# Kernel tuning notes

Hardware: AMD Instinct MI355X
Metric: run time of the kernel (lower is better)

The kernel has to match this reference:

```python
import jax, jax.numpy as jnp
import numpy as np

B, T, D = 2, 2048, 2048
N_HEAD, N_KV_HEAD = 16, 4
HEAD_DIM = D // N_HEAD  # 128
N_REP = N_HEAD // N_KV_HEAD  # 4
ROPE_THETA = 10000.0
EPS = float(jnp.finfo(jnp.float32).eps)  # torch.nn.RMSNorm default eps


def setup_inputs() -> dict:
    key = jax.random.key(0)
    ks = jax.random.split(key, 6)
    s = 0.02
    return {
        "x": jax.random.normal(ks[0], (B, T, D), jnp.float32),
        "wq": jax.random.normal(ks[1], (N_HEAD * HEAD_DIM, D), jnp.float32) * s,
        "wk": jax.random.normal(ks[2], (N_KV_HEAD * HEAD_DIM, D), jnp.float32) * s,
        "wv": jax.random.normal(ks[3], (N_KV_HEAD * HEAD_DIM, D), jnp.float32) * s,
        "wo": jax.random.normal(ks[4], (D, D), jnp.float32) * s,
        "q_norm_w": jnp.ones((HEAD_DIM,), jnp.float32),
        "k_norm_w": jnp.ones((HEAD_DIM,), jnp.float32),
    }


def _rope(x):
    # x: (B, T, H, hd). Llama/Qwen complex-pair RoPE on consecutive pairs.
    t = x.shape[1]
    hd = x.shape[-1]
    inv_freq = 1.0 / (ROPE_THETA ** (jnp.arange(0, hd, 2, dtype=jnp.float32) / hd))
    ang = jnp.arange(t, dtype=jnp.float32)[:, None] * inv_freq[None, :]  # (T, hd/2)
    cos = jnp.cos(ang)[None, :, None, :]
    sin = jnp.sin(ang)[None, :, None, :]
    xr = x[..., 0::2]
    xi = x[..., 1::2]
    or_ = xr * cos - xi * sin
    oi_ = xr * sin + xi * cos
    return jnp.stack([or_, oi_], axis=-1).reshape(x.shape)


def _rmsnorm(x, w):
    var = jnp.mean(jnp.square(x), axis=-1, keepdims=True)
    return x * jax.lax.rsqrt(var + EPS) * w


def reference(x, wq, wk, wv, wo, q_norm_w, k_norm_w):
    b, t, d = x.shape
    xq = (x @ wq.T).reshape(b, t, N_HEAD, HEAD_DIM)
    xk = (x @ wk.T).reshape(b, t, N_KV_HEAD, HEAD_DIM)
    xv = (x @ wv.T).reshape(b, t, N_KV_HEAD, HEAD_DIM)
    xq = _rope(xq)
    xk = _rope(xk)
    # repeat_kv: (B,T,KV,hd) -> (B,T,KV*n_rep,hd)
    xk = jnp.repeat(xk, N_REP, axis=2)
    xv = jnp.repeat(xv, N_REP, axis=2)
    # (B, H, T, hd)
    xq = xq.transpose(0, 2, 1, 3)
    xk = xk.transpose(0, 2, 1, 3)
    xv = xv.transpose(0, 2, 1, 3)
    xq = _rmsnorm(xq, q_norm_w)
    xk = _rmsnorm(xk, k_norm_w)
    scale = 1.0 / np.sqrt(HEAD_DIM)
    scores = jnp.einsum("bhqd,bhkd->bhqk", xq, xk) * scale
    causal = jnp.tril(jnp.ones((t, t), bool))
    scores = jnp.where(causal[None, None], scores, -jnp.inf)
    attn = jax.nn.softmax(scores, axis=-1)
    y = jnp.einsum("bhqk,bhkd->bhqd", attn, xv)
    y = y.transpose(0, 2, 1, 3).reshape(b, t, d)
    return y @ wo.T
```

## Files before the change

kernel.cpp:

```cpp
#include <hip/hip_runtime.h>
#include <hip/hip_bf16.h>
#include <math.h>

typedef __attribute__((ext_vector_type(8))) short bf16x8;
typedef __attribute__((ext_vector_type(4))) float f32x4;
typedef __attribute__((ext_vector_type(4))) unsigned int u32x4;

#define DEV static __device__ __forceinline__

constexpr int TT   = 2048;
constexpr int DDIM = 2048;
constexpr int QKVN = 3072;
constexpr int MROWS = 4096;
constexpr float RSCALE = 0.08838834764831845f;
constexpr float LOG2E  = 1.4426950408889634f;
constexpr float SC2    = RSCALE * LOG2E;
constexpr float REPS   = 1.1920928955078125e-07f;

DEV unsigned short f2b(float f) {
  union { float f; unsigned int u; } v; v.f = f;
  unsigned int u = v.u;
  return (unsigned short)((u + 0x7fffu + ((u >> 16) & 1u)) >> 16);
}
DEV float b2f(unsigned short h) {
  union { unsigned int u; float f; } v; v.u = ((unsigned int)h) << 16;
  return v.f;
}
DEV f32x4 mfma16(bf16x8 a, bf16x8 b, f32x4 c) {
  return __builtin_amdgcn_mfma_f32_16x16x32_bf16(a, b, c, 0, 0, 0);
}
DEV void gload_lds16(const void* g, void* l) {
  __builtin_amdgcn_global_load_lds(
      (const __attribute__((address_space(1))) unsigned int*)g,
      (__attribute__((address_space(3))) unsigned int*)l, 16, 0, 0);
}

__global__ __launch_bounds__(256) void cvt_kernel(const float* __restrict__ in,
                                                  unsigned short* __restrict__ out,
                                                  int n4) {
  int i = blockIdx.x * 256 + threadIdx.x;
  if (i < n4) {
    float4 v = ((const float4*)in)[i];
    ushort4 o;
    o.x = f2b(v.x); o.y = f2b(v.y); o.z = f2b(v.z); o.w = f2b(v.w);
    ((ushort4*)out)[i] = o;
  }
}

template <typename CT>
__global__ __launch_bounds__(256) void gemm_bt(const unsigned short* __restrict__ A,
                                               const unsigned short* __restrict__ B,
                                               CT* __restrict__ C,
                                               int M, int N, int K) {
  __shared__ unsigned short As[128 * 32];
  __shared__ unsigned short Bs[128 * 32];
  const int tid = threadIdx.x;
  const int l = tid & 63, w = tid >> 6;
  const int wr = w >> 1, wc = w & 1;
  const long bm = (long)blockIdx.y * 128, bn = (long)blockIdx.x * 128;

  const int r0 = tid >> 2;
  const int c0 = (tid & 3) * 8;
  const unsigned short* Ag0 = A + (bm + r0) * (long)K + c0;
  const unsigned short* Ag1 = A + (bm + r0 + 64) * (long)K + c0;
  const unsigned short* Bg0 = B + (bn + r0) * (long)K + c0;
  const unsigned short* Bg1 = B + (bn + r0 + 64) * (long)K + c0;
  char* lA = (char*)As + w * 1024;
  char* lB = (char*)Bs + w * 1024;

  f32x4 acc[4][4];
#pragma unroll
  for (int m = 0; m < 4; ++m)
#pragma unroll
    for (int n = 0; n < 4; ++n) acc[m][n] = f32x4{0.f, 0.f, 0.f, 0.f};

  const int lr = l & 15;
  const int lk = (l >> 4) * 8;

  for (int k0 = 0; k0 < K; k0 += 32) {
    gload_lds16(Ag0 + k0, lA);
    gload_lds16(Ag1 + k0, lA + 4096);
    gload_lds16(Bg0 + k0, lB);
    gload_lds16(Bg1 + k0, lB + 4096);
    __syncthreads();
    bf16x8 af[4], bfr[4];
#pragma unroll
    for (int m = 0; m < 4; ++m)
      af[m] = *(const bf16x8*)(As + (wr * 64 + m * 16 + lr) * 32 + lk);
#pragma unroll
    for (int n = 0; n < 4; ++n)
      bfr[n] = *(const bf16x8*)(Bs + (wc * 64 + n * 16 + lr) * 32 + lk);
#pragma unroll
    for (int m = 0; m < 4; ++m)
#pragma unroll
      for (int n = 0; n < 4; ++n)
        acc[m][n] = mfma16(af[m], bfr[n], acc[m][n]);
    __syncthreads();
  }

#pragma unroll
  for (int m = 0; m < 4; ++m)
#pragma unroll
    for (int n = 0; n < 4; ++n)
#pragma unroll
      for (int r = 0; r < 4; ++r) {
        long row = bm + wr * 64 + m * 16 + (l >> 4) * 4 + r;
        long col = bn + wc * 64 + n * 16 + (l & 15);
        float val = acc[m][n][r];
        if constexpr (sizeof(CT) == 2)
          ((unsigned short*)C)[row * N + col] = f2b(val);
        else
          ((float*)C)[row * N + col] = val;
      }
}

__global__ __launch_bounds__(256) void rope_norm_kernel(unsigned short* __restrict__ qkv,
                                                        const float* __restrict__ qw,
                                                        const float* __restrict__ kw) {
  const int slot = blockIdx.x * 4 + (threadIdx.x >> 6);
  const int l = threadIdx.x & 63;
  const int bt = slot / 20;
  const int hs = slot - bt * 20;
  const int t = bt & (TT - 1);
  const bool isq = hs < 16;
  const int col0 = isq ? hs * 128 : 2048 + (hs - 16) * 128;
  const float* w = isq ? qw : kw;
  unsigned short* p = qkv + (long)bt * QKVN + col0;

  unsigned int pr = *(const unsigned int*)(p + 2 * l);
  float xr = b2f((unsigned short)(pr & 0xffffu));
  float xi = b2f((unsigned short)(pr >> 16));

  float ang = (float)t * exp2f(-0.207620509f * (float)l);
  float s = sinf(ang), c = cosf(ang);
  float orr = xr * c - xi * s;
  float oii = xr * s + xi * c;

  float ss = orr * orr + oii * oii;
#pragma unroll
  for (int d = 1; d < 64; d <<= 1) ss += __shfl_xor(ss, d);
  float sc = rsqrtf(ss * (1.f / 128.f) + REPS);

  unsigned int outw = ((unsigned int)f2b(oii * sc * w[2 * l + 1]) << 16) |
                      (unsigned int)f2b(orr * sc * w[2 * l]);
  *(unsigned int*)(p + 2 * l) = outw;
}

__global__ __launch_bounds__(256) void fattn_kernel(const unsigned short* __restrict__ qkv,
                                                    unsigned short* __restrict__ y) {
  const int qb = (int)gridDim.x - 1 - (int)blockIdx.x;
  const int bh = blockIdx.y;
  const int b = bh >> 4, h = bh & 15;
  const unsigned short* base = qkv + (long)b * TT * QKVN;
  const unsigned short* Qp = base + h * 128;
  const unsigned short* Kp = base + 2048 + (h >> 2) * 128;
  const unsigned short* Vp = base + 2560 + (h >> 2) * 128;
  const int tid = threadIdx.x;
  const int l = tid & 63, w = tid >> 6;
  const int lr = l & 15, lg = l >> 4;
  const int qrow = qb * 64 + w * 16;

  __shared__ char KsB[2][16384];
  __shared__ char VtB[2][16384];
  __shared__ unsigned short Ps[4][16][72];

  bf16x8 qf[4];
  {
    const unsigned short* qp = Qp + (long)(qrow + lr) * QKVN + lg * 8;
#pragma unroll
    for (int c = 0; c < 4; ++c) qf[c] = *(const bf16x8*)(qp + c * 32);
  }

  const int krow0 = tid >> 4;
  const int kcolb = ((tid & 15) * 16) ^ ((krow0 & 7) << 4);
  const unsigned short* Kg = Kp + (long)krow0 * QKVN + (kcolb >> 1);
  const int vm = tid & 15;
  const unsigned short* Vg = Vp + (long)(tid >> 4) * QKVN + vm * 8;
  int vwoff[8];
#pragma unroll
  for (int j = 0; j < 8; ++j) {
    int d = vm * 8 + j;
    vwoff[j] = d * 128 + (((((d >> 1) ^ (d >> 3)) & 7) << 4));
  }
  const int lgk = ((lr & 7) << 4);

  f32x4 o[8];
#pragma unroll
  for (int n = 0; n < 8; ++n) o[n] = f32x4{0.f, 0.f, 0.f, 0.f};
  float mrow[4], lsum[4];
#pragma unroll
  for (int r = 0; r < 4; ++r) { mrow[r] = -__builtin_inff(); lsum[r] = 0.f; }

  const int ntiles = qb + 1;
  u32x4 vr[4];

  {
    char* kdst = KsB[0] + (w * 64) * 16;
#pragma unroll
    for (int i = 0; i < 4; ++i)
      gload_lds16(Kg + (long)16 * i * QKVN, kdst + i * 4096);
#pragma unroll
    for (int i = 0; i < 4; ++i)
      vr[i] = *(const u32x4*)(Vg + (long)16 * i * QKVN);
    asm volatile("s_waitcnt vmcnt(0)" ::: "memory");
    char* vt = VtB[0];
#pragma unroll
    for (int i = 0; i < 4; ++i) {
      int kv2 = 2 * ((tid >> 4) + 16 * i);
      const unsigned short* tv = (const unsigned short*)&vr[i];
#pragma unroll
      for (int j = 0; j < 8; ++j) {
        int base128 = (vm * 8 + j) * 128;
        int swz = vwoff[j] - base128;
        *(unsigned short*)(vt + base128 + (kv2 ^ swz)) = tv[j];
      }
    }
    asm volatile("s_waitcnt lgkmcnt(0)" ::: "memory");
    __builtin_amdgcn_s_barrier();
  }

  int cur = 0;
  for (int it = 0; it < ntiles; ++it) {
    const int kv0 = it * 64;
    const int nxt = cur ^ 1;
    const bool pfn = (it + 1 < ntiles);

    if (pfn) {
      const long adv = (long)(it + 1) * 64 * QKVN;
      char* kdst = KsB[nxt] + (w * 64) * 16;
#pragma unroll
      for (int i = 0; i < 4; ++i)
        gload_lds16(Kg + adv + (long)16 * i * QKVN, kdst + i * 4096);
#pragma unroll
      for (int i = 0; i < 4; ++i)
        vr[i] = *(const u32x4*)(Vg + adv + (long)16 * i * QKVN);
    }

    const char* KsC = KsB[cur];
    const char* VtC = VtB[cur];
    f32x4 sb[4];
#pragma unroll
    for (int kb = 0; kb < 4; ++kb) {
      if (kv0 + kb * 16 <= qrow + 15) {
        f32x4 s = f32x4{0.f, 0.f, 0.f, 0.f};
#pragma unroll
        for (int c = 0; c < 4; ++c) {
          bf16x8 kf = *(const bf16x8*)(KsC + (kb * 16 + lr) * 256 +
                                       ((16 * lg + 64 * c) ^ lgk));
          s = mfma16(qf[c], kf, s);
        }
        sb[kb] = s;
      } else {
        sb[kb] = f32x4{-__builtin_inff(), -__builtin_inff(),
                       -__builtin_inff(), -__builtin_inff()};
      }
    }

    float rmax[4];
#pragma unroll
    for (int r = 0; r < 4; ++r) rmax[r] = -__builtin_inff();
#pragma unroll
    for (int kb = 0; kb < 4; ++kb) {
      int kcol = kv0 + kb * 16 + lr;
#pragma unroll
      for (int r = 0; r < 4; ++r) {
        int qr = qrow + lg * 4 + r;
        if (kcol > qr) sb[kb][r] = -__builtin_inff();
        rmax[r] = fmaxf(rmax[r], sb[kb][r]);
      }
    }
#pragma unroll
    for (int r = 0; r < 4; ++r)
#pragma unroll
      for (int d = 1; d < 16; d <<= 1)
        rmax[r] = fmaxf(rmax[r], __shfl_xor(rmax[r], d));

    float alpha[4];
#pragma unroll
    for (int r = 0; r < 4; ++r) {
      float mn = fmaxf(mrow[r], rmax[r] * SC2);
      alpha[r] = exp2f(mrow[r] - mn);
      mrow[r] = mn;
    }
    float rsum[4] = {0.f, 0.f, 0.f, 0.f};
#pragma unroll
    for (int kb = 0; kb < 4; ++kb)
#pragma unroll
      for (int r = 0; r < 4; ++r) {
        float pv = exp2f(sb[kb][r] * SC2 - mrow[r]);
        rsum[r] += pv;
        Ps[w][lg * 4 + r][kb * 16 + lr] = f2b(pv);
      }
#pragma unroll
    for (int r = 0; r < 4; ++r) {
#pragma unroll
      for (int d = 1; d < 16; d <<= 1) rsum[r] += __shfl_xor(rsum[r], d);
      lsum[r] = lsum[r] * alpha[r] + rsum[r];
    }
#pragma unroll
    for (int n = 0; n < 8; ++n)
#pragma unroll
      for (int r = 0; r < 4; ++r) o[n][r] *= alpha[r];

    asm volatile("s_waitcnt lgkmcnt(0)" ::: "memory");
    __builtin_amdgcn_sched_barrier(0);

#pragma unroll
    for (int kc = 0; kc < 2; ++kc) {
      if (kv0 + kc * 32 <= qrow + 15) {
        bf16x8 pf = *(const bf16x8*)(&Ps[w][lr][kc * 32 + lg * 8]);
#pragma unroll
        for (int n = 0; n < 8; ++n) {
          int d = n * 16 + lr;
          int swz = (((d >> 1) ^ (d >> 3)) & 7) << 4;
          bf16x8 vf = *(const bf16x8*)(VtC + d * 128 +
                                       ((kc * 64 + 16 * lg) ^ swz));
          o[n] = mfma16(pf, vf, o[n]);
        }
      }
    }

    if (pfn) {
      asm volatile("s_waitcnt vmcnt(0)" ::: "memory");
      char* vt = VtB[nxt];
#pragma unroll
      for (int i = 0; i < 4; ++i) {
        int kv2 = 2 * ((tid >> 4) + 16 * i);
        const unsigned short* tv = (const unsigned short*)&vr[i];
#pragma unroll
        for (int j = 0; j < 8; ++j) {
          int base128 = (vm * 8 + j) * 128;
          int swz = vwoff[j] - base128;
          *(unsigned short*)(vt + base128 + (kv2 ^ swz)) = tv[j];
        }
      }
      asm volatile("s_waitcnt lgkmcnt(0)" ::: "memory");
      __builtin_amdgcn_s_barrier();
    }
    cur = nxt;
  }

  float inv[4];
#pragma unroll
  for (int r = 0; r < 4; ++r) inv[r] = 1.f / lsum[r];
  unsigned short* yp = y + (long)(b * TT + qrow) * DDIM + h * 128;
#pragma unroll
  for (int n = 0; n < 8; ++n)
#pragma unroll
    for (int r = 0; r < 4; ++r)
      yp[(long)(lg * 4 + r) * DDIM + n * 16 + lr] = f2b(o[n][r] * inv[r]);
}

extern "C" void kernel_launch(void* const* d_in, const int* in_sizes, int n_in,
                              void* d_out, int out_size, void* d_ws, size_t ws_size,
                              hipStream_t stream) {
  const float* x  = (const float*)d_in[0];
  const float* wq = (const float*)d_in[1];
  const float* wk = (const float*)d_in[2];
  const float* wv = (const float*)d_in[3];
  const float* wo = (const float*)d_in[4];
  const float* qw = (const float*)d_in[5];
  const float* kw = (const float*)d_in[6];
  float* out = (float*)d_out;

  unsigned short* xb   = (unsigned short*)d_ws;
  unsigned short* wcat = xb + (size_t)MROWS * DDIM;
  unsigned short* wob  = wcat + (size_t)QKVN * DDIM;
  unsigned short* qkv  = wob + (size_t)DDIM * DDIM;
  unsigned short* yb   = qkv + (size_t)MROWS * QKVN;

  auto cvt = [&](const float* src, unsigned short* dst, long n) {
    int n4 = (int)(n / 4);
    cvt_kernel<<<(n4 + 255) / 256, 256, 0, stream>>>(src, dst, n4);
  };
  cvt(x,  xb,   (long)MROWS * DDIM);
  cvt(wq, wcat,                         (long)2048 * 2048);
  cvt(wk, wcat + (size_t)2048 * 2048,   (long)512 * 2048);
  cvt(wv, wcat + (size_t)2560 * 2048,   (long)512 * 2048);
  cvt(wo, wob,  (long)2048 * 2048);

  dim3 g1(QKVN / 128, MROWS / 128);
  gemm_bt<unsigned short><<<g1, 256, 0, stream>>>(xb, wcat, qkv, MROWS, QKVN, DDIM);

  rope_norm_kernel<<<(MROWS * 20) / 4, 256, 0, stream>>>(qkv, qw, kw);

  dim3 g2(TT / 64, 32);
  fattn_kernel<<<g2, 256, 0, stream>>>(qkv, yb);

  dim3 g3(DDIM / 128, MROWS / 128);
  gemm_bt<float><<<g3, 256, 0, stream>>>(yb, wob, out, MROWS, DDIM, DDIM);
}
```

Measured before the change: 491.2 us.

## Double-buffer GEMM LDS and restructure flash attention with paired blocks and transposed scores

The GEMM now double-buffers its A/B LDS tiles, so the next K slice is prefetched while MFMAs run on the current one, at the cost of twice the shared memory. The attention kernel pairs a short and a long causal query block in each workgroup (grid 16x32) to balance work. It computes S transposed so P stays in registers and feeds the PV MFMA without an LDS round trip. It also adds a lazy rescale that skips the output rescaling unless the row max grows by more than 8 in log2 units, packed bf16 conversion, and s_setprio around the MFMA sections. Together these aim to cut LDS traffic, barrier stalls and load imbalance, but they make the kernel considerably more complex.

```diff
diff --git a/kernel.cpp b/kernel.cpp
--- a/kernel.cpp
+++ b/kernel.cpp
@@ -5,6 +5,7 @@
 typedef __attribute__((ext_vector_type(8))) short bf16x8;
 typedef __attribute__((ext_vector_type(4))) float f32x4;
 typedef __attribute__((ext_vector_type(4))) unsigned int u32x4;
+typedef __attribute__((ext_vector_type(2))) unsigned int u32x2;
 
 #define DEV static __device__ __forceinline__
 
@@ -34,6 +35,12 @@
       (const __attribute__((address_space(1))) unsigned int*)g,
       (__attribute__((address_space(3))) unsigned int*)l, 16, 0, 0);
 }
+DEV unsigned int cvtpk(float lo, float hi) {
+  unsigned int r;
+  asm("v_cvt_pk_bf16_f32 %0, %1, %2" : "=v"(r) : "v"(lo), "v"(hi));
+  return r;
+}
+union PB { u32x4 u; bf16x8 b; };
 
 __global__ __launch_bounds__(256) void cvt_kernel(const float* __restrict__ in,
                                                   unsigned short* __restrict__ out,
@@ -52,8 +59,8 @@
                                                const unsigned short* __restrict__ B,
                                                CT* __restrict__ C,
                                                int M, int N, int K) {
-  __shared__ unsigned short As[128 * 32];
-  __shared__ unsigned short Bs[128 * 32];
+  __shared__ unsigned short As[2][128 * 32];
+  __shared__ unsigned short Bs[2][128 * 32];
   const int tid = threadIdx.x;
   const int l = tid & 63, w = tid >> 6;
   const int wr = w >> 1, wc = w & 1;
@@ -65,8 +72,6 @@
   const unsigned short* Ag1 = A + (bm + r0 + 64) * (long)K + c0;
   const unsigned short* Bg0 = B + (bn + r0) * (long)K + c0;
   const unsigned short* Bg1 = B + (bn + r0 + 64) * (long)K + c0;
-  char* lA = (char*)As + w * 1024;
-  char* lB = (char*)Bs + w * 1024;
 
   f32x4 acc[4][4];
 #pragma unroll
@@ -77,25 +82,42 @@
   const int lr = l & 15;
   const int lk = (l >> 4) * 8;
 
+  {
+    char* lA = (char*)(As[0]) + w * 1024;
+    char* lB = (char*)(Bs[0]) + w * 1024;
+    gload_lds16(Ag0, lA);
+    gload_lds16(Ag1, lA + 4096);
+    gload_lds16(Bg0, lB);
+    gload_lds16(Bg1, lB + 4096);
+  }
+  __syncthreads();
+
+  int cur = 0;
   for (int k0 = 0; k0 < K; k0 += 32) {
-    gload_lds16(Ag0 + k0, lA);
-    gload_lds16(Ag1 + k0, lA + 4096);
-    gload_lds16(Bg0 + k0, lB);
-    gload_lds16(Bg1 + k0, lB + 4096);
-    __syncthreads();
+    if (k0 + 32 < K) {
+      char* lA = (char*)(As[cur ^ 1]) + w * 1024;
+      char* lB = (char*)(Bs[cur ^ 1]) + w * 1024;
+      gload_lds16(Ag0 + k0 + 32, lA);
+      gload_lds16(Ag1 + k0 + 32, lA + 4096);
+      gload_lds16(Bg0 + k0 + 32, lB);
+      gload_lds16(Bg1 + k0 + 32, lB + 4096);
+    }
+    const unsigned short* Asc = As[cur];
+    const unsigned short* Bsc = Bs[cur];
     bf16x8 af[4], bfr[4];
 #pragma unroll
     for (int m = 0; m < 4; ++m)
-      af[m] = *(const bf16x8*)(As + (wr * 64 + m * 16 + lr) * 32 + lk);
+      af[m] = *(const bf16x8*)(Asc + (wr * 64 + m * 16 + lr) * 32 + lk);
 #pragma unroll
     for (int n = 0; n < 4; ++n)
-      bfr[n] = *(const bf16x8*)(Bs + (wc * 64 + n * 16 + lr) * 32 + lk);
+      bfr[n] = *(const bf16x8*)(Bsc + (wc * 64 + n * 16 + lr) * 32 + lk);
 #pragma unroll
     for (int m = 0; m < 4; ++m)
 #pragma unroll
       for (int n = 0; n < 4; ++n)
         acc[m][n] = mfma16(af[m], bfr[n], acc[m][n]);
     __syncthreads();
+    cur ^= 1;
   }
 
 #pragma unroll
@@ -148,7 +170,7 @@
 
 __global__ __launch_bounds__(256) void fattn_kernel(const unsigned short* __restrict__ qkv,
                                                     unsigned short* __restrict__ y) {
-  const int qb = (int)gridDim.x - 1 - (int)blockIdx.x;
+  const int bx = blockIdx.x;
   const int bh = blockIdx.y;
   const int b = bh >> 4, h = bh & 15;
   const unsigned short* base = qkv + (long)b * TT * QKVN;
@@ -158,197 +180,204 @@
   const int tid = threadIdx.x;
   const int l = tid & 63, w = tid >> 6;
   const int lr = l & 15, lg = l >> 4;
-  const int qrow = qb * 64 + w * 16;
 
   __shared__ char KsB[2][16384];
   __shared__ char VtB[2][16384];
-  __shared__ unsigned short Ps[4][16][72];
-
-  bf16x8 qf[4];
-  {
-    const unsigned short* qp = Qp + (long)(qrow + lr) * QKVN + lg * 8;
-#pragma unroll
-    for (int c = 0; c < 4; ++c) qf[c] = *(const bf16x8*)(qp + c * 32);
-  }
 
   const int krow0 = tid >> 4;
   const int kcolb = ((tid & 15) * 16) ^ ((krow0 & 7) << 4);
   const unsigned short* Kg = Kp + (long)krow0 * QKVN + (kcolb >> 1);
   const int vm = tid & 15;
   const unsigned short* Vg = Vp + (long)(tid >> 4) * QKVN + vm * 8;
-  int vwoff[8];
-#pragma unroll
-  for (int j = 0; j < 8; ++j) {
-    int d = vm * 8 + j;
-    vwoff[j] = d * 128 + (((((d >> 1) ^ (d >> 3)) & 7) << 4));
-  }
   const int lgk = ((lr & 7) << 4);
 
-  f32x4 o[8];
-#pragma unroll
-  for (int n = 0; n < 8; ++n) o[n] = f32x4{0.f, 0.f, 0.f, 0.f};
-  float mrow[4], lsum[4];
-#pragma unroll
-  for (int r = 0; r < 4; ++r) { mrow[r] = -__builtin_inff(); lsum[r] = 0.f; }
-
-  const int ntiles = qb + 1;
-  u32x4 vr[4];
-
-  {
-    char* kdst = KsB[0] + (w * 64) * 16;
-#pragma unroll
-    for (int i = 0; i < 4; ++i)
-      gload_lds16(Kg + (long)16 * i * QKVN, kdst + i * 4096);
-#pragma unroll
-    for (int i = 0; i < 4; ++i)
-      vr[i] = *(const u32x4*)(Vg + (long)16 * i * QKVN);
-    asm volatile("s_waitcnt vmcnt(0)" ::: "memory");
-    char* vt = VtB[0];
-#pragma unroll
-    for (int i = 0; i < 4; ++i) {
-      int kv2 = 2 * ((tid >> 4) + 16 * i);
-      const unsigned short* tv = (const unsigned short*)&vr[i];
-#pragma unroll
-      for (int j = 0; j < 8; ++j) {
-        int base128 = (vm * 8 + j) * 128;
-        int swz = vwoff[j] - base128;
-        *(unsigned short*)(vt + base128 + (kv2 ^ swz)) = tv[j];
-      }
+  for (int seg = 0; seg < 2; ++seg) {
+    const int qb = seg ? bx : (31 - bx);
+    const int qrow = qb * 64 + w * 16;
+    const int ntiles = qb + 1;
+
+    bf16x8 qf[4];
+    {
+      const unsigned short* qp = Qp + (long)(qrow + lr) * QKVN + lg * 8;
+#pragma unroll
+      for (int c = 0; c < 4; ++c) qf[c] = *(const bf16x8*)(qp + c * 32);
     }
-    asm volatile("s_waitcnt lgkmcnt(0)" ::: "memory");
-    __builtin_amdgcn_s_barrier();
-  }
-
-  int cur = 0;
-  for (int it = 0; it < ntiles; ++it) {
-    const int kv0 = it * 64;
-    const int nxt = cur ^ 1;
-    const bool pfn = (it + 1 < ntiles);
-
-    if (pfn) {
-      const long adv = (long)(it + 1) * 64 * QKVN;
-      char* kdst = KsB[nxt] + (w * 64) * 16;
+
+    f32x4 o[8];
+#pragma unroll
+    for (int n = 0; n < 8; ++n) o[n] = f32x4{0.f, 0.f, 0.f, 0.f};
+    float m = -__builtin_inff(), lsum = 0.f;
+
+    __syncthreads();
+
+    u32x4 vr[4];
+    {
+      char* kdst = KsB[0] + (w * 64) * 16;
 #pragma unroll
       for (int i = 0; i < 4; ++i)
-        gload_lds16(Kg + adv + (long)16 * i * QKVN, kdst + i * 4096);
+        gload_lds16(Kg + (long)16 * i * QKVN, kdst + i * 4096);
 #pragma unroll
       for (int i = 0; i < 4; ++i)
-        vr[i] = *(const u32x4*)(Vg + adv + (long)16 * i * QKVN);
-    }
-
-    const char* KsC = KsB[cur];
-    const char* VtC = VtB[cur];
-    f32x4 sb[4];
-#pragma unroll
-    for (int kb = 0; kb < 4; ++kb) {
-      if (kv0 + kb * 16 <= qrow + 15) {
-        f32x4 s = f32x4{0.f, 0.f, 0.f, 0.f};
-#pragma unroll
-        for (int c = 0; c < 4; ++c) {
-          bf16x8 kf = *(const bf16x8*)(KsC + (kb * 16 + lr) * 256 +
-                                       ((16 * lg + 64 * c) ^ lgk));
-          s = mfma16(qf[c], kf, s);
-        }
-        sb[kb] = s;
-      } else {
-        sb[kb] = f32x4{-__builtin_inff(), -__builtin_inff(),
-                       -__builtin_inff(), -__builtin_inff()};
-      }
-    }
-
-    float rmax[4];
-#pragma unroll
-    for (int r = 0; r < 4; ++r) rmax[r] = -__builtin_inff();
-#pragma unroll
-    for (int kb = 0; kb < 4; ++kb) {
-      int kcol = kv0 + kb * 16 + lr;
-#pragma unroll
-      for (int r = 0; r < 4; ++r) {
-        int qr = qrow + lg * 4 + r;
-        if (kcol > qr) sb[kb][r] = -__builtin_inff();
-        rmax[r] = fmaxf(rmax[r], sb[kb][r]);
-      }
-    }
-#pragma unroll
-    for (int r = 0; r < 4; ++r)
-#pragma unroll
-      for (int d = 1; d < 16; d <<= 1)
-        rmax[r] = fmaxf(rmax[r], __shfl_xor(rmax[r], d));
-
-    float alpha[4];
-#pragma unroll
-    for (int r = 0; r < 4; ++r) {
-      float mn = fmaxf(mrow[r], rmax[r] * SC2);
-      alpha[r] = exp2f(mrow[r] - mn);
-      mrow[r] = mn;
-    }
-    float rsum[4] = {0.f, 0.f, 0.f, 0.f};
-#pragma unroll
-    for (int kb = 0; kb < 4; ++kb)
-#pragma unroll
-      for (int r = 0; r < 4; ++r) {
-        float pv = exp2f(sb[kb][r] * SC2 - mrow[r]);
-        rsum[r] += pv;
-        Ps[w][lg * 4 + r][kb * 16 + lr] = f2b(pv);
-      }
-#pragma unroll
-    for (int r = 0; r < 4; ++r) {
-#pragma unroll
-      for (int d = 1; d < 16; d <<= 1) rsum[r] += __shfl_xor(rsum[r], d);
-      lsum[r] = lsum[r] * alpha[r] + rsum[r];
-    }
-#pragma unroll
-    for (int n = 0; n < 8; ++n)
-#pragma unroll
-      for (int r = 0; r < 4; ++r) o[n][r] *= alpha[r];
-
-    asm volatile("s_waitcnt lgkmcnt(0)" ::: "memory");
-    __builtin_amdgcn_sched_barrier(0);
-
-#pragma unroll
-    for (int kc = 0; kc < 2; ++kc) {
-      if (kv0 + kc * 32 <= qrow + 15) {
-        bf16x8 pf = *(const bf16x8*)(&Ps[w][lr][kc * 32 + lg * 8]);
-#pragma unroll
-        for (int n = 0; n < 8; ++n) {
-          int d = n * 16 + lr;
-          int swz = (((d >> 1) ^ (d >> 3)) & 7) << 4;
-          bf16x8 vf = *(const bf16x8*)(VtC + d * 128 +
-                                       ((kc * 64 + 16 * lg) ^ swz));
-          o[n] = mfma16(pf, vf, o[n]);
-        }
-      }
-    }
-
-    if (pfn) {
+        vr[i] = *(const u32x4*)(Vg + (long)16 * i * QKVN);
       asm volatile("s_waitcnt vmcnt(0)" ::: "memory");
-      char* vt = VtB[nxt];
+      char* vt = VtB[0];
 #pragma unroll
       for (int i = 0; i < 4; ++i) {
         int kv2 = 2 * ((tid >> 4) + 16 * i);
         const unsigned short* tv = (const unsigned short*)&vr[i];
 #pragma unroll
         for (int j = 0; j < 8; ++j) {
-          int base128 = (vm * 8 + j) * 128;
-          int swz = vwoff[j] - base128;
-          *(unsigned short*)(vt + base128 + (kv2 ^ swz)) = tv[j];
+          int d = vm * 8 + j;
+          int swz = (((d >> 1) ^ (d >> 3)) & 7) << 4;
+          *(unsigned short*)(vt + d * 128 + (kv2 ^ swz)) = tv[j];
         }
       }
       asm volatile("s_waitcnt lgkmcnt(0)" ::: "memory");
+      __builtin_amdgcn_sched_barrier(0);
       __builtin_amdgcn_s_barrier();
     }
-    cur = nxt;
+
+    int cur = 0;
+    for (int it = 0; it < ntiles; ++it) {
+      const int kv0 = it * 64;
+      const int nxt = cur ^ 1;
+      const bool pfn = (it + 1 < ntiles);
+
+      if (pfn) {
+        const long adv = (long)(it + 1) * 64 * QKVN;
+        char* kdst = KsB[nxt] + (w * 64) * 16;
+#pragma unroll
+        for (int i = 0; i < 4; ++i)
+          gload_lds16(Kg + adv + (long)16 * i * QKVN, kdst + i * 4096);
+#pragma unroll
+        for (int i = 0; i < 4; ++i)
+          vr[i] = *(const u32x4*)(Vg + adv + (long)16 * i * QKVN);
+      }
+
+      const char* KsC = KsB[cur];
+      const char* VtC = VtB[cur];
+
+      f32x4 sT[4];
+      __builtin_amdgcn_s_setprio(1);
+#pragma unroll
+      for (int kb = 0; kb < 4; ++kb) {
+        if (kv0 + kb * 16 <= qrow + 15) {
+          f32x4 s = f32x4{0.f, 0.f, 0.f, 0.f};
+#pragma unroll
+          for (int c = 0; c < 4; ++c) {
+            bf16x8 kf = *(const bf16x8*)(KsC + (kb * 16 + lr) * 256 +
+                                         ((16 * lg + 64 * c) ^ lgk));
+            s = mfma16(kf, qf[c], s);
+          }
+          sT[kb] = s;
+        } else {
+          sT[kb] = f32x4{-__builtin_inff(), -__builtin_inff(),
+                         -__builtin_inff(), -__builtin_inff()};
+        }
+      }
+      __builtin_amdgcn_s_setprio(0);
+
+      if (kv0 + 48 >= qrow) {
+#pragma unroll
+        for (int kb = 0; kb < 4; ++kb)
+#pragma unroll
+          for (int r = 0; r < 4; ++r) {
+            int ks = kv0 + kb * 16 + 4 * lg + r;
+            sT[kb][r] = (ks > qrow + lr) ? -__builtin_inff() : sT[kb][r];
+          }
+      }
+
+      float pmax = -__builtin_inff();
+#pragma unroll
+      for (int kb = 0; kb < 4; ++kb)
+#pragma unroll
+        for (int r = 0; r < 4; ++r) pmax = fmaxf(pmax, sT[kb][r]);
+      pmax = fmaxf(pmax, __shfl_xor(pmax, 16));
+      pmax = fmaxf(pmax, __shfl_xor(pmax, 32));
+      pmax *= SC2;
+
+      if (!__all(pmax <= m + 8.f)) {
+        float mn = fmaxf(m, pmax);
+        float al = exp2f(m - mn);
+        m = mn;
+        lsum *= al;
+        float ao[4];
+#pragma unroll
+        for (int r = 0; r < 4; ++r) ao[r] = __shfl(al, 20 * lg + r);
+#pragma unroll
+        for (int n = 0; n < 8; ++n)
+#pragma unroll
+          for (int r = 0; r < 4; ++r) o[n][r] *= ao[r];
+      }
+
+      float rs = 0.f;
+      unsigned int pk[4][2];
+#pragma unroll
+      for (int kb = 0; kb < 4; ++kb) {
+        float p0 = exp2f(sT[kb][0] * SC2 - m);
+        float p1 = exp2f(sT[kb][1] * SC2 - m);
+        float p2 = exp2f(sT[kb][2] * SC2 - m);
+        float p3 = exp2f(sT[kb][3] * SC2 - m);
+        rs += (p0 + p1) + (p2 + p3);
+        pk[kb][0] = cvtpk(p0, p1);
+        pk[kb][1] = cvtpk(p2, p3);
+      }
+      rs += __shfl_xor(rs, 16);
+      rs += __shfl_xor(rs, 32);
+      lsum += rs;
+
+      __builtin_amdgcn_s_setprio(1);
+#pragma unroll
+      for (int c = 0; c < 2; ++c) {
+        if (kv0 + c * 32 <= qrow + 15) {
+          PB pb;
+          pb.u = u32x4{pk[2 * c][0], pk[2 * c][1], pk[2 * c + 1][0], pk[2 * c + 1][1]};
+#pragma unroll
+          for (int n = 0; n < 8; ++n) {
+            int d = n * 16 + lr;
+            int gsw = (((d >> 1) ^ (d >> 3)) & 7) << 4;
+            const char* vb = VtC + d * 128;
+            u32x2 vlo = *(const u32x2*)(vb + ((64 * c + 8 * lg) ^ gsw));
+            u32x2 vhi = *(const u32x2*)(vb + ((64 * c + 32 + 8 * lg) ^ gsw));
+            PB vv; vv.u = u32x4{vlo[0], vlo[1], vhi[0], vhi[1]};
+            o[n] = mfma16(pb.b, vv.b, o[n]);
+          }
+        }
+      }
+      __builtin_amdgcn_s_setprio(0);
+
+      if (pfn) {
+        asm volatile("s_waitcnt vmcnt(0)" ::: "memory");
+        char* vt = VtB[nxt];
+#pragma unroll
+        for (int i = 0; i < 4; ++i) {
+          int kv2 = 2 * ((tid >> 4) + 16 * i);
+          const unsigned short* tv = (const unsigned short*)&vr[i];
+#pragma unroll
+          for (int j = 0; j < 8; ++j) {
+            int d = vm * 8 + j;
+            int swz = (((d >> 1) ^ (d >> 3)) & 7) << 4;
+            *(unsigned short*)(vt + d * 128 + (kv2 ^ swz)) = tv[j];
+          }
+        }
+        asm volatile("s_waitcnt lgkmcnt(0)" ::: "memory");
+        __builtin_amdgcn_sched_barrier(0);
+        __builtin_amdgcn_s_barrier();
+      }
+      cur = nxt;
+    }
+
+    float inv = 1.f / lsum;
+    float io[4];
+#pragma unroll
+    for (int r = 0; r < 4; ++r) io[r] = __shfl(inv, 20 * lg + r);
+    unsigned short* yp = y + (long)(b * TT + qrow) * DDIM + h * 128;
+#pragma unroll
+    for (int n = 0; n < 8; ++n)
+#pragma unroll
+      for (int r = 0; r < 4; ++r)
+        yp[(long)(lg * 4 + r) * DDIM + n * 16 + lr] = f2b(o[n][r] * io[r]);
   }
-
-  float inv[4];
-#pragma unroll
-  for (int r = 0; r < 4; ++r) inv[r] = 1.f / lsum[r];
-  unsigned short* yp = y + (long)(b * TT + qrow) * DDIM + h * 128;
-#pragma unroll
-  for (int n = 0; n < 8; ++n)
-#pragma unroll
-    for (int r = 0; r < 4; ++r)
-      yp[(long)(lg * 4 + r) * DDIM + n * 16 + lr] = f2b(o[n][r] * inv[r]);
 }
 
 extern "C" void kernel_launch(void* const* d_in, const int* in_sizes, int n_in,
@@ -384,7 +413,7 @@
 
   rope_norm_kernel<<<(MROWS * 20) / 4, 256, 0, stream>>>(qkv, qw, kw);
 
-  dim3 g2(TT / 64, 32);
+  dim3 g2(16, 32);
   fattn_kernel<<<g2, 256, 0, stream>>>(qkv, yb);
 
   dim3 g3(DDIM / 128, MROWS / 128);
```

Result: faster. 421.1 us (-14.3%).
